# Performance work log

Measured on AMD Instinct MI355X. Metric: run time of the kernel, lower is better.

Reference implementation:

```python
import jax, jax.numpy as jnp
import numpy as np

B, T, D = 16, 2048, 1024

def setup_inputs() -> dict:
    key = jax.random.key(0)
    k1, k2 = jax.random.split(key)
    xs = jax.random.normal(k1, (B, T, D), dtype=jnp.float32)
    xs_len = jnp.maximum(jax.random.randint(k2, (B,), 0, T + 1), 1).astype(jnp.int64)
    return {"xs": xs, "xs_len": xs_len}

def reference(xs, xs_len):
    # masked mean over time: equivalent to mean(x[:x_len], axis=0) per sample
    T_ = xs.shape[1]
    mask = (jnp.arange(T_)[None, :] < xs_len[:, None]).astype(xs.dtype)  # [B, T]
    summed = jnp.einsum('btd,bt->bd', xs, mask)                          # [B, D]
    return summed / xs_len.astype(xs.dtype)[:, None]
```

## Files before the change

### kernel.cpp

```cpp
#include <hip/hip_runtime.h>


#define B_ 16
#define T_ 2048
#define D_ 1024
#define CH 32
#define NS (T_ / CH)

__device__ __forceinline__ long long read_len(const void* len_ptr, int b)
{
    long long len;
    const long long v0 = ((const long long*)len_ptr)[0];
    if (v0 >= 1 && v0 <= (long long)T_) {
        len = ((const long long*)len_ptr)[b];
    } else {
        len = (long long)((const int*)len_ptr)[b];
    }
    if (len < 1) len = 1;
    if (len > T_) len = T_;
    return len;
}

__global__ __launch_bounds__(256) void mp_partial(
    const float* __restrict__ xs,
    const void* __restrict__ len_ptr,
    float* __restrict__ ws)
{
    const int bid = blockIdx.x;
    const int b = bid >> 6;
    const int s = bid & (NS - 1);

    const long long len = read_len(len_ptr, b);

    const int t0 = s * CH;
    int tend = t0 + CH;
    if ((long long)tend > len) tend = (int)len;
    if (t0 >= tend) return;

    const int tid = threadIdx.x;

    const float4* src = (const float4*)xs + ((long)b * T_ + t0) * (D_ / 4) + tid;
    float4 acc = make_float4(0.f, 0.f, 0.f, 0.f);

    #pragma unroll 4
    for (int t = t0; t < tend; ++t) {
        float4 v = *src;
        src += (D_ / 4);
        acc.x += v.x; acc.y += v.y; acc.z += v.z; acc.w += v.w;
    }

    ((float4*)ws)[(long)bid * (D_ / 4) + tid] = acc;
}

__global__ __launch_bounds__(256) void mp_reduce(
    const float* __restrict__ ws,
    const void* __restrict__ len_ptr,
    float* __restrict__ out)
{
    const int b = blockIdx.x >> 2;
    const int c = blockIdx.x & 3;
    const int lane = threadIdx.x & 63;
    const int w = threadIdx.x >> 6;

    const long long len = read_len(len_ptr, b);
    const int nact = (int)((len + (CH - 1)) >> 5);

    const int d4 = c * 64 + lane;
    const float4* wsp = (const float4*)ws;

    float4 acc = make_float4(0.f, 0.f, 0.f, 0.f);
    #pragma unroll 4
    for (int s = w; s < nact; s += 4) {
        float4 v = wsp[(long)(b * NS + s) * (D_ / 4) + d4];
        acc.x += v.x; acc.y += v.y; acc.z += v.z; acc.w += v.w;
    }

    __shared__ float4 sm[4][64];
    sm[w][lane] = acc;
    __syncthreads();

    if (w == 0) {
        float4 a0 = sm[0][lane], a1 = sm[1][lane], a2 = sm[2][lane], a3 = sm[3][lane];
        const float inv = 1.0f / (float)len;
        float4 r;
        r.x = (a0.x + a1.x + a2.x + a3.x) * inv;
        r.y = (a0.y + a1.y + a2.y + a3.y) * inv;
        r.z = (a0.z + a1.z + a2.z + a3.z) * inv;
        r.w = (a0.w + a1.w + a2.w + a3.w) * inv;
        ((float4*)out)[(long)b * (D_ / 4) + d4] = r;
    }
}

extern "C" void kernel_launch(void* const* d_in, const int* in_sizes, int n_in,
                              void* d_out, int out_size, void* d_ws, size_t ws_size,
                              hipStream_t stream)
{
    const float* xs = (const float*)d_in[0];
    const void* xs_len = d_in[1];
    float* out = (float*)d_out;
    float* ws = (float*)d_ws;

    mp_partial<<<dim3(B_ * NS), dim3(256), 0, stream>>>(xs, xs_len, ws);
    mp_reduce<<<dim3(B_ * 4), dim3(256), 0, stream>>>(ws, xs_len, out);
}
```

Before: 22.45 us.

## Balance time-chunk work across blocks proportional to sequence lengths

```diff
diff --git a/kernel.cpp b/kernel.cpp
--- a/kernel.cpp
+++ b/kernel.cpp
@@ -4,21 +4,35 @@
 #define B_ 16
 #define T_ 2048
 #define D_ 1024
-#define CH 32
-#define NS (T_ / CH)
+#define NB 1024
 
-__device__ __forceinline__ long long read_len(const void* len_ptr, int b)
+__device__ __forceinline__ void read_lens(const void* len_ptr, int* lens)
 {
-    long long len;
     const long long v0 = ((const long long*)len_ptr)[0];
-    if (v0 >= 1 && v0 <= (long long)T_) {
-        len = ((const long long*)len_ptr)[b];
-    } else {
-        len = (long long)((const int*)len_ptr)[b];
+    const bool is64 = (v0 >= 1 && v0 <= (long long)T_);
+    #pragma unroll
+    for (int b = 0; b < B_; ++b) {
+        long long len = is64 ? ((const long long*)len_ptr)[b]
+                             : (long long)((const int*)len_ptr)[b];
+        if (len < 1) len = 1;
+        if (len > T_) len = T_;
+        lens[b] = (int)len;
     }
-    if (len < 1) len = 1;
-    if (len > T_) len = T_;
-    return len;
+}
+
+__device__ __forceinline__ void partition(const int* lens, int* cnt, int* pref)
+{
+    int total = 0;
+    #pragma unroll
+    for (int b = 0; b < B_; ++b) total += lens[b];
+    int p = 0;
+    #pragma unroll
+    for (int b = 0; b < B_; ++b) {
+        pref[b] = p;
+        cnt[b] = (lens[b] * NB + total - 1) / total;
+        p += cnt[b];
+    }
+    pref[B_] = p;
 }
 
 __global__ __launch_bounds__(256) void mp_partial(
@@ -26,24 +40,31 @@
     const void* __restrict__ len_ptr,
     float* __restrict__ ws)
 {
+    int lens[B_], cnt[B_], pref[B_ + 1];
+    read_lens(len_ptr, lens);
+    partition(lens, cnt, pref);
+
     const int bid = blockIdx.x;
-    const int b = bid >> 6;
-    const int s = bid & (NS - 1);
+    if (bid >= pref[B_]) return;
 
-    const long long len = read_len(len_ptr, b);
-
-    const int t0 = s * CH;
-    int tend = t0 + CH;
-    if ((long long)tend > len) tend = (int)len;
-    if (t0 >= tend) return;
+    int b = 0;
+    #pragma unroll
+    for (int k = 0; k < B_; ++k) {
+        if (bid >= pref[k + 1]) b = k + 1;
+    }
+    const int j = bid - pref[b];
+    const int len = lens[b];
+    const int cb = cnt[b];
+    const int r0 = (int)((long)j * len / cb);
+    const int r1 = (int)((long)(j + 1) * len / cb);
 
     const int tid = threadIdx.x;
 
-    const float4* src = (const float4*)xs + ((long)b * T_ + t0) * (D_ / 4) + tid;
+    const float4* src = (const float4*)xs + ((long)b * T_ + r0) * (D_ / 4) + tid;
     float4 acc = make_float4(0.f, 0.f, 0.f, 0.f);
 
     #pragma unroll 4
-    for (int t = t0; t < tend; ++t) {
+    for (int t = r0; t < r1; ++t) {
         float4 v = *src;
         src += (D_ / 4);
         acc.x += v.x; acc.y += v.y; acc.z += v.z; acc.w += v.w;
@@ -57,21 +78,24 @@
     const void* __restrict__ len_ptr,
     float* __restrict__ out)
 {
+    int lens[B_], cnt[B_], pref[B_ + 1];
+    read_lens(len_ptr, lens);
+    partition(lens, cnt, pref);
+
     const int b = blockIdx.x >> 2;
     const int c = blockIdx.x & 3;
     const int lane = threadIdx.x & 63;
     const int w = threadIdx.x >> 6;
 
-    const long long len = read_len(len_ptr, b);
-    const int nact = (int)((len + (CH - 1)) >> 5);
+    const int s0 = pref[b];
+    const int s1 = pref[b + 1];
 
     const int d4 = c * 64 + lane;
     const float4* wsp = (const float4*)ws;
 
     float4 acc = make_float4(0.f, 0.f, 0.f, 0.f);
-    #pragma unroll 4
-    for (int s = w; s < nact; s += 4) {
-        float4 v = wsp[(long)(b * NS + s) * (D_ / 4) + d4];
+    for (int s = s0 + w; s < s1; s += 4) {
+        float4 v = wsp[(long)s * (D_ / 4) + d4];
         acc.x += v.x; acc.y += v.y; acc.z += v.z; acc.w += v.w;
     }
 
@@ -81,7 +105,7 @@
 
     if (w == 0) {
         float4 a0 = sm[0][lane], a1 = sm[1][lane], a2 = sm[2][lane], a3 = sm[3][lane];
-        const float inv = 1.0f / (float)len;
+        const float inv = 1.0f / (float)lens[b];
         float4 r;
         r.x = (a0.x + a1.x + a2.x + a3.x) * inv;
         r.y = (a0.y + a1.y + a2.y + a3.y) * inv;
@@ -100,6 +124,6 @@
     float* out = (float*)d_out;
     float* ws = (float*)d_ws;
 
-    mp_partial<<<dim3(B_ * NS), dim3(256), 0, stream>>>(xs, xs_len, ws);
+    mp_partial<<<dim3(NB + B_), dim3(256), 0, stream>>>(xs, xs_len, ws);
     mp_reduce<<<dim3(B_ * 4), dim3(256), 0, stream>>>(ws, xs_len, out);
 }
```

Measured after the change: 31.30 us. 1.39x slower.

## Use persistent blocks with atomic ticket work-stealing and unrolled chunk loads

Applied to the files above, without the earlier changes.

```diff
diff --git a/kernel.cpp b/kernel.cpp
--- a/kernel.cpp
+++ b/kernel.cpp
@@ -5,55 +5,96 @@
 #define T_ 2048
 #define D_ 1024
 #define CH 32
-#define NS (T_ / CH)
+#define NSL 1024
+#define G1 256
+#define TAKES (NSL / G1)
+#define SLOT0_F4 64
 
-__device__ __forceinline__ long long read_len(const void* len_ptr, int b)
+__device__ __forceinline__ bool sniff64(const void* p)
 {
-    long long len;
-    const long long v0 = ((const long long*)len_ptr)[0];
-    if (v0 >= 1 && v0 <= (long long)T_) {
-        len = ((const long long*)len_ptr)[b];
-    } else {
-        len = (long long)((const int*)len_ptr)[b];
-    }
+    const long long v0 = ((const long long*)p)[0];
+    return (v0 >= 1 && v0 <= (long long)T_);
+}
+
+__device__ __forceinline__ int load_len(const void* p, bool is64, int k)
+{
+    long long len = is64 ? ((const long long*)p)[k]
+                         : (long long)((const int*)p)[k];
     if (len < 1) len = 1;
     if (len > T_) len = T_;
-    return len;
+    return (int)len;
 }
 
 __global__ __launch_bounds__(256) void mp_partial(
     const float* __restrict__ xs,
     const void* __restrict__ len_ptr,
-    float* __restrict__ ws)
+    unsigned* __restrict__ ctr,
+    float4* __restrict__ ws)
 {
-    const int bid = blockIdx.x;
-    const int b = bid >> 6;
-    const int s = bid & (NS - 1);
+    const int tid = threadIdx.x;
+    const bool is64 = sniff64(len_ptr);
 
-    const long long len = read_len(len_ptr, b);
+    unsigned t_next = (tid == 0) ? 0u : 0u;
+    __shared__ unsigned sh_ticket;
+    if (tid == 0) sh_ticket = atomicAdd(ctr, 1u);
+    __syncthreads();
+    t_next = sh_ticket;
 
-    const int t0 = s * CH;
-    int tend = t0 + CH;
-    if ((long long)tend > len) tend = (int)len;
-    if (t0 >= tend) return;
+    #pragma unroll 1
+    for (int i = 0; i < TAKES; ++i) {
+        const unsigned ticket = t_next;
+        if (i + 1 < TAKES) {
+            __syncthreads();
+            if (tid == 0) sh_ticket = atomicAdd(ctr, 1u);
+        }
 
-    const int tid = threadIdx.x;
+        const int s  = (int)(ticket & (NSL - 1));
+        const int b  = s >> 6;
+        const int sl = s & 63;
+        const int len = load_len(len_ptr, is64, b);
+        const int t0 = sl * CH;
 
-    const float4* src = (const float4*)xs + ((long)b * T_ + t0) * (D_ / 4) + tid;
-    float4 acc = make_float4(0.f, 0.f, 0.f, 0.f);
+        if (t0 < len) {
+            const float4* src = (const float4*)xs + ((long)b * T_ + t0) * (D_ / 4) + tid;
+            float4 acc = make_float4(0.f, 0.f, 0.f, 0.f);
 
-    #pragma unroll 4
-    for (int t = t0; t < tend; ++t) {
-        float4 v = *src;
-        src += (D_ / 4);
-        acc.x += v.x; acc.y += v.y; acc.z += v.z; acc.w += v.w;
+            if (t0 + CH <= len) {
+                #pragma unroll 1
+                for (int r = 0; r < CH; r += 8) {
+                    float4 v0 = src[0 * (D_ / 4)];
+                    float4 v1 = src[1 * (D_ / 4)];
+                    float4 v2 = src[2 * (D_ / 4)];
+                    float4 v3 = src[3 * (D_ / 4)];
+                    float4 v4 = src[4 * (D_ / 4)];
+                    float4 v5 = src[5 * (D_ / 4)];
+                    float4 v6 = src[6 * (D_ / 4)];
+                    float4 v7 = src[7 * (D_ / 4)];
+                    src += 8 * (D_ / 4);
+                    acc.x += v0.x + v1.x + v2.x + v3.x + v4.x + v5.x + v6.x + v7.x;
+                    acc.y += v0.y + v1.y + v2.y + v3.y + v4.y + v5.y + v6.y + v7.y;
+                    acc.z += v0.z + v1.z + v2.z + v3.z + v4.z + v5.z + v6.z + v7.z;
+                    acc.w += v0.w + v1.w + v2.w + v3.w + v4.w + v5.w + v6.w + v7.w;
+                }
+            } else {
+                const int n = len - t0;
+                for (int t = 0; t < n; ++t) {
+                    float4 v = *src;
+                    src += (D_ / 4);
+                    acc.x += v.x; acc.y += v.y; acc.z += v.z; acc.w += v.w;
+                }
+            }
+            ws[SLOT0_F4 + (long)s * (D_ / 4) + tid] = acc;
+        }
+
+        if (i + 1 < TAKES) {
+            __syncthreads();
+            t_next = sh_ticket;
+        }
     }
-
-    ((float4*)ws)[(long)bid * (D_ / 4) + tid] = acc;
 }
 
 __global__ __launch_bounds__(256) void mp_reduce(
-    const float* __restrict__ ws,
+    const float4* __restrict__ ws,
     const void* __restrict__ len_ptr,
     float* __restrict__ out)
 {
@@ -62,16 +103,16 @@
     const int lane = threadIdx.x & 63;
     const int w = threadIdx.x >> 6;
 
-    const long long len = read_len(len_ptr, b);
-    const int nact = (int)((len + (CH - 1)) >> 5);
+    const bool is64 = sniff64(len_ptr);
+    const int len = load_len(len_ptr, is64, b);
+    const int nact = (len + CH - 1) >> 5;
 
     const int d4 = c * 64 + lane;
-    const float4* wsp = (const float4*)ws;
 
     float4 acc = make_float4(0.f, 0.f, 0.f, 0.f);
     #pragma unroll 4
     for (int s = w; s < nact; s += 4) {
-        float4 v = wsp[(long)(b * NS + s) * (D_ / 4) + d4];
+        float4 v = ws[SLOT0_F4 + (long)(b * 64 + s) * (D_ / 4) + d4];
         acc.x += v.x; acc.y += v.y; acc.z += v.z; acc.w += v.w;
     }
 
@@ -98,8 +139,9 @@
     const float* xs = (const float*)d_in[0];
     const void* xs_len = d_in[1];
     float* out = (float*)d_out;
-    float* ws = (float*)d_ws;
+    unsigned* ctr = (unsigned*)d_ws;
+    float4* ws = (float4*)d_ws;
 
-    mp_partial<<<dim3(B_ * NS), dim3(256), 0, stream>>>(xs, xs_len, ws);
+    mp_partial<<<dim3(G1), dim3(256), 0, stream>>>(xs, xs_len, ctr, ws);
     mp_reduce<<<dim3(B_ * 4), dim3(256), 0, stream>>>(ws, xs_len, out);
 }
```

Result: slower. 32.81 us (+46.2%).
